# Performance work log

Hardware: AMD Instinct MI355X
Metric: run time of the kernel (lower is better)

## Reference

```python
import jax, jax.numpy as jnp
import numpy as np

DEPTH = 6
HIDDEN = 1152
INTER = 4304
HEADS = 16
HEAD_DIM = HIDDEN // HEADS  # 72
NUM_IMAGES = 4
GH = 32
GW = 32
MERGE = 2
SEQ = NUM_IMAGES * GH * GW  # 4096, cu_seqlens = [0,1024,2048,3072,4096]
OUT_HIDDEN = 2048
NPOS_SIDE = 48
PATCH_DIM = 3 * 2 * 16 * 16  # 1536
DS_IDX = (2, 4)
EPS = 1e-6
SCALE = HEAD_DIM ** -0.5
MERGED = HIDDEN * MERGE * MERGE  # 4608


def _block_order(h, w, m):
    # token order that groups m x m spatial-merge blocks contiguously
    return np.arange(h * w).reshape(h // m, m, w // m, m).transpose(0, 2, 1, 3).reshape(-1)

_ORDER = _block_order(GH, GW, MERGE)


def _rope_cos_sin():
    hpos = _ORDER // GW
    wpos = _ORDER % GW
    half = HEAD_DIM // 2
    inv = 1.0 / (10000.0 ** (np.arange(0, half, 2, dtype=np.float32) / half))
    fr = np.arange(max(GH, GW), dtype=np.float32)[:, None] * inv[None, :]
    r = np.concatenate([fr[hpos], fr[wpos]], axis=-1)  # (GH*GW, head_dim//2)
    emb = np.tile(np.concatenate([r, r], axis=-1), (NUM_IMAGES, 1))  # (SEQ, HEAD_DIM)
    return jnp.asarray(np.cos(emb)), jnp.asarray(np.sin(emb))


def _pos_interp():
    # static bilinear-interp gather indices/weights: 48x48 grid -> (GH,GW), block order
    n = NPOS_SIDE
    hl = np.linspace(0, n - 1, GH); wl = np.linspace(0, n - 1, GW)
    h0 = np.floor(hl).astype(np.int64); h1 = np.minimum(h0 + 1, n - 1); dh = (hl - h0).astype(np.float32)
    w0 = np.floor(wl).astype(np.int64); w1 = np.minimum(w0 + 1, n - 1); dw = (wl - w0).astype(np.float32)
    idx = np.stack([(h0[:, None] * n + w0[None, :]).reshape(-1),
                    (h0[:, None] * n + w1[None, :]).reshape(-1),
                    (h1[:, None] * n + w0[None, :]).reshape(-1),
                    (h1[:, None] * n + w1[None, :]).reshape(-1)], 0)
    wgt = np.stack([((1 - dh)[:, None] * (1 - dw)[None, :]).reshape(-1),
                    ((1 - dh)[:, None] * dw[None, :]).reshape(-1),
                    (dh[:, None] * (1 - dw)[None, :]).reshape(-1),
                    (dh[:, None] * dw[None, :]).reshape(-1)], 0).astype(np.float32)
    return idx[:, _ORDER], wgt[:, _ORDER]

_PIDX, _PWGT = _pos_interp()


def _ln(x, g, b):
    mu = x.mean(-1, keepdims=True)
    var = ((x - mu) ** 2).mean(-1, keepdims=True)
    return (x - mu) * jax.lax.rsqrt(var + EPS) * g + b


def _rot_half(x):
    x1, x2 = jnp.split(x, 2, axis=-1)
    return jnp.concatenate([-x2, x1], axis=-1)


def _attention(x, qkv_w, qkv_b, proj_w, proj_b, cos, sin):
    qkv = (x @ qkv_w.T + qkv_b).reshape(SEQ, 3, HEADS, HEAD_DIM)
    q, k, v = qkv[:, 0], qkv[:, 1], qkv[:, 2]
    c, s = cos[:, None, :], sin[:, None, :]
    q = q * c + _rot_half(q) * s
    k = k * c + _rot_half(k) * s
    # equal-length cu_seqlens chunks -> batched block-diagonal attention
    qb = q.reshape(NUM_IMAGES, -1, HEADS, HEAD_DIM)
    kb = k.reshape(NUM_IMAGES, -1, HEADS, HEAD_DIM)
    vb = v.reshape(NUM_IMAGES, -1, HEADS, HEAD_DIM)
    att = jax.nn.softmax(jnp.einsum('bqhd,bkhd->bhqk', qb, kb) * SCALE, axis=-1)
    o = jnp.einsum('bhqk,bkhd->bqhd', att, vb).reshape(SEQ, HIDDEN)
    return o @ proj_w.T + proj_b


def _merger(x, g, b, f1w, f1b, f2w, f2b, post):
    if post:
        h = _ln(x.reshape(-1, MERGED), g, b)
    else:
        h = _ln(x, g, b).reshape(-1, MERGED)
    h = jax.nn.gelu(h @ f1w.T + f1b, approximate=True)
    return h @ f2w.T + f2b


def setup_inputs():
    key = jax.random.key(0)
    ks = iter(jax.random.split(key, 40))
    def w(shape, scale=0.02):
        return jax.random.normal(next(ks), shape, jnp.float32) * scale
    return {
        'pixel_values': jax.random.normal(next(ks), (SEQ, PATCH_DIM), jnp.float32),
        'patch_w': w((HIDDEN, PATCH_DIM)), 'patch_b': w((HIDDEN,)),
        'pos_embed': w((NPOS_SIDE * NPOS_SIDE, HIDDEN)),
        'qkv_w': w((DEPTH, 3 * HIDDEN, HIDDEN)), 'qkv_b': w((DEPTH, 3 * HIDDEN)),
        'proj_w': w((DEPTH, HIDDEN, HIDDEN)), 'proj_b': w((DEPTH, HIDDEN)),
        'ln1_g': jnp.ones((DEPTH, HIDDEN)), 'ln1_b': jnp.zeros((DEPTH, HIDDEN)),
        'ln2_g': jnp.ones((DEPTH, HIDDEN)), 'ln2_b': jnp.zeros((DEPTH, HIDDEN)),
        'fc1_w': w((DEPTH, INTER, HIDDEN)), 'fc1_b': w((DEPTH, INTER)),
        'fc2_w': w((DEPTH, HIDDEN, INTER)), 'fc2_b': w((DEPTH, HIDDEN)),
        'm_ln_g': jnp.ones((HIDDEN,)), 'm_ln_b': jnp.zeros((HIDDEN,)),
        'm_fc1_w': w((MERGED, MERGED)), 'm_fc1_b': w((MERGED,)),
        'm_fc2_w': w((OUT_HIDDEN, MERGED)), 'm_fc2_b': w((OUT_HIDDEN,)),
        'ds_ln_g': jnp.ones((2, MERGED)), 'ds_ln_b': jnp.zeros((2, MERGED)),
        'ds_fc1_w': w((2, MERGED, MERGED)), 'ds_fc1_b': w((2, MERGED)),
        'ds_fc2_w': w((2, OUT_HIDDEN, MERGED)), 'ds_fc2_b': w((2, OUT_HIDDEN)),
    }


def reference(pixel_values, patch_w, patch_b, pos_embed, qkv_w, qkv_b, proj_w, proj_b,
              ln1_g, ln1_b, ln2_g, ln2_b, fc1_w, fc1_b, fc2_w, fc2_b,
              m_ln_g, m_ln_b, m_fc1_w, m_fc1_b, m_fc2_w, m_fc2_b,
              ds_ln_g, ds_ln_b, ds_fc1_w, ds_fc1_b, ds_fc2_w, ds_fc2_b):
    cos, sin = _rope_cos_sin()
    # patch embed: stride==kernel Conv3d == flat linear on (C*T*P*P)
    x = pixel_values @ patch_w.T + patch_b  # (SEQ, HIDDEN)
    pe = (pos_embed[jnp.asarray(_PIDX)] * jnp.asarray(_PWGT)[..., None]).sum(0)
    x = x + jnp.tile(pe, (NUM_IMAGES, 1))
    ds = []
    for i in range(DEPTH):
        x = x + _attention(_ln(x, ln1_g[i], ln1_b[i]), qkv_w[i], qkv_b[i], proj_w[i], proj_b[i], cos, sin)
        h = _ln(x, ln2_g[i], ln2_b[i])
        x = x + (jax.nn.gelu(h @ fc1_w[i].T + fc1_b[i], approximate=True) @ fc2_w[i].T + fc2_b[i])
        if i in DS_IDX:
            j = DS_IDX.index(i)
            ds.append(_merger(x, ds_ln_g[j], ds_ln_b[j], ds_fc1_w[j], ds_fc1_b[j], ds_fc2_w[j], ds_fc2_b[j], post=True))
    out = _merger(x, m_ln_g, m_ln_b, m_fc1_w, m_fc1_b, m_fc2_w, m_fc2_b, post=False)
    return (out, ds[0], ds[1])
```

## Files before the change

### kernel.cpp

```cpp
#include <hip/hip_runtime.h>
#include <hip/hip_bf16.h>
#include <math.h>

typedef __hip_bfloat16 bf16;
typedef __attribute__((ext_vector_type(8))) __bf16 bfv8;
typedef __attribute__((ext_vector_type(4))) __bf16 bfv4;
typedef __attribute__((ext_vector_type(4))) float float4v;

__device__ inline float bf2f(bf16 v) { return __bfloat162float(v); }
__device__ inline bf16 f2bf(float v) { return __float2bfloat16(v); }

__device__ inline float gelu_f(float v) {
  return 0.5f * v * (1.f + tanhf(0.7978845608028654f * (v + 0.044715f * v * v * v)));
}

__global__ void dtype_probe(const unsigned* __restrict__ g, int* __restrict__ flag) {
  *flag = (*g == 0x3F800000u) ? 1 : 0;
}

__device__ inline float loadf_dyn(const void* p, long i, int isf32) {
  return isf32 ? ((const float*)p)[i] : bf2f(((const bf16*)p)[i]);
}

__global__ __launch_bounds__(256) void cvt_bf16(const void* __restrict__ src,
                                                long off, __bf16* __restrict__ dst,
                                                long n, const int* __restrict__ flagp) {
  const long i = ((long)blockIdx.x * 256 + threadIdx.x) * 8;
  if (i >= n) return;
  if (*flagp) {
    const float* sp = (const float*)src + off + i;
    float4v a = *(const float4v*)sp;
    float4v b = *(const float4v*)(sp + 4);
    bfv8 r;
    r[0] = (__bf16)a[0]; r[1] = (__bf16)a[1];
    r[2] = (__bf16)a[2]; r[3] = (__bf16)a[3];
    r[4] = (__bf16)b[0]; r[5] = (__bf16)b[1];
    r[6] = (__bf16)b[2]; r[7] = (__bf16)b[3];
    *(bfv8*)(dst + i) = r;
  } else {
    *(bfv8*)(dst + i) = *(const bfv8*)((const __bf16*)src + off + i);
  }
}

__device__ inline void cp16(const __bf16* g, __bf16* l) {
  __builtin_amdgcn_global_load_lds(
      (const __attribute__((address_space(1))) void*)g,
      (__attribute__((address_space(3))) void*)l, 16, 0, 0);
}

template <int EPI>
__global__ __launch_bounds__(256) void gemm_bt(
    const void* __restrict__ Av, const void* __restrict__ Wv,
    const void* __restrict__ Bv, void* __restrict__ Cv,
    const int* __restrict__ flagp, int M, int N, int K, int lda, int ldw,
    int ldc, long sA, long sW, long sC, long a0, long w0, long b0, long c0,
    int ksplit, float scale) {
  __shared__ __align__(16) __bf16 As[128 * 32];
  __shared__ __align__(16) __bf16 Ws[128 * 32];
  const int tid = threadIdx.x;
  const int bz = blockIdx.z;

  const int nx = gridDim.x;
  const int nwg = nx * gridDim.y;
  const int orig = blockIdx.y * nx + blockIdx.x;
  const int xcd = orig & 7, lid = orig >> 3, qq = nwg >> 3, rr = nwg & 7;
  const int wg = (xcd < rr ? xcd * (qq + 1) : rr * (qq + 1) + (xcd - rr) * qq) + lid;
  const int bm = (wg / nx) * 128;
  const int bn = (wg % nx) * 128;

  int kof = 0, klen = K;
  if (ksplit > 0) {
    kof = bz * ksplit;
    klen = min(ksplit, K - kof);
  }
  const __bf16* Ap = (const __bf16*)Av + a0 + (size_t)bz * sA + kof;
  const __bf16* Wp = (const __bf16*)Wv + w0 + (size_t)bz * sW + kof;

  const int lane = tid & 63, wid = tid >> 6;
  const int wm = (wid >> 1) * 64, wn = (wid & 1) * 64;
  const int q = lane >> 4, lm = lane & 15;

  const int sr = lane >> 2;
  const int sc = (lane & 3) * 8;
  const int ar = bm + wid * 32 + sr;
  const int wr = bn + wid * 32 + sr;
  const size_t aoff0 = (size_t)(ar < M ? ar : M - 1) * lda + sc;
  const size_t aoff1 = (size_t)(ar + 16 < M ? ar + 16 : M - 1) * lda + sc;
  const size_t woff0 = (size_t)(wr < N ? wr : N - 1) * ldw + sc;
  const size_t woff1 = (size_t)(wr + 16 < N ? wr + 16 : N - 1) * ldw + sc;
  __bf16* lA = &As[wid * 32 * 32];
  __bf16* lW = &Ws[wid * 32 * 32];

  float4v acc[4][4];
#pragma unroll
  for (int i = 0; i < 4; i++)
#pragma unroll
    for (int j = 0; j < 4; j++) acc[i][j] = (float4v)0.f;

  auto compute = [&]() {
    bfv8 af[4], wf[4];
#pragma unroll
    for (int i = 0; i < 4; i++) {
      af[i] = *(const bfv8*)&As[(wm + i * 16 + lm) * 32 + q * 8];
      wf[i] = *(const bfv8*)&Ws[(wn + i * 16 + lm) * 32 + q * 8];
    }
#pragma unroll
    for (int i = 0; i < 4; i++)
#pragma unroll
      for (int j = 0; j < 4; j++)
        acc[i][j] = __builtin_amdgcn_mfma_f32_16x16x32_bf16(af[i], wf[j],
                                                            acc[i][j], 0, 0, 0);
  };

  const int nfull = klen >> 5;
  for (int kt = 0; kt < nfull; ++kt) {
    const int k0 = kt << 5;
    cp16(Ap + aoff0 + k0, lA);
    cp16(Ap + aoff1 + k0, lA + 512);
    cp16(Wp + woff0 + k0, lW);
    cp16(Wp + woff1 + k0, lW + 512);
    __syncthreads();
    compute();
    __syncthreads();
  }

  const int kr = klen & 31;
  if (kr) {
    const int k0 = nfull << 5;
    const int r0 = tid >> 2, ce = (tid & 3) * 8;
#pragma unroll
    for (int it = 0; it < 2; ++it) {
      const int r = r0 + it * 64;
      const int gm = bm + r, gn = bn + r;
      bfv8 av = (bfv8)(__bf16)0.f;
      if (ce < kr && gm < M) av = *(const bfv8*)(Ap + (size_t)gm * lda + k0 + ce);
      *(bfv8*)&As[r * 32 + ce] = av;
      bfv8 wv = (bfv8)(__bf16)0.f;
      if (ce < kr && gn < N) wv = *(const bfv8*)(Wp + (size_t)gn * ldw + k0 + ce);
      *(bfv8*)&Ws[r * 32 + ce] = wv;
    }
    __syncthreads();
    compute();
  }

  const int isf32 = *flagp;
  float* Cf = (float*)Cv;
  bf16* Cb = (bf16*)Cv;
  const size_t cbase = (size_t)c0 + (size_t)bz * sC;
#pragma unroll
  for (int i = 0; i < 4; i++) {
#pragma unroll
    for (int j = 0; j < 4; j++) {
      const int col = bn + wn + j * 16 + lm;
      if (col >= N) continue;
      float bv = 0.f;
      if (EPI != 4 && Bv) bv = loadf_dyn(Bv, b0 + col, isf32);
#pragma unroll
      for (int r = 0; r < 4; r++) {
        const int rowg = bm + wm + i * 16 + q * 4 + r;
        if (rowg >= M) continue;
        float v = acc[i][j][r] + bv;
        const size_t off = cbase + (size_t)rowg * ldc + col;
        if (EPI == 0) {
          Cb[off] = f2bf(v);
        } else if (EPI == 1) {
          Cb[off] = f2bf(gelu_f(v));
        } else if (EPI == 3) {
          Cf[off] = v;
        } else if (EPI == 4) {
          Cf[off] = v * scale;
        }
      }
    }
  }
}

template <int MODE>
__global__ __launch_bounds__(256) void reduce_add(
    const float* __restrict__ part, long slab, int S,
    const void* __restrict__ bias, long b0, void* __restrict__ outv, long c0,
    long n, int N, const int* __restrict__ flagp) {
  const int isf32 = *flagp;
  const long i4 = ((long)blockIdx.x * 256 + threadIdx.x) * 4;
  if (i4 >= n) return;
  float4v s = *(const float4v*)(part + i4);
  for (int t = 1; t < S; ++t) s += *(const float4v*)(part + (size_t)t * slab + i4);
  const int col = (int)(i4 % N);
#pragma unroll
  for (int u = 0; u < 4; ++u) s[u] += loadf_dyn(bias, b0 + col + u, isf32);
  if (MODE == 0) {
    *(float4v*)((float*)outv + i4) = s;
  } else if (MODE == 1) {
    float4v x0 = *(const float4v*)((float*)outv + i4);
    *(float4v*)((float*)outv + i4) = x0 + s;
  } else if (MODE == 2) {
    bfv4 r;
#pragma unroll
    for (int u = 0; u < 4; ++u) r[u] = (__bf16)gelu_f(s[u]);
    *(bfv4*)((bf16*)outv + i4) = r;
  } else {
    if (isf32) {
      *(float4v*)((float*)outv + c0 + i4) = s;
    } else {
      bfv4 r;
#pragma unroll
      for (int u = 0; u < 4; ++u) r[u] = (__bf16)s[u];
      *(bfv4*)((bf16*)outv + c0 + i4) = r;
    }
  }
}

__global__ __launch_bounds__(256) void ln_rows(const float* __restrict__ x,
                                               const void* __restrict__ g,
                                               const void* __restrict__ b,
                                               long gboff, bf16* __restrict__ out,
                                               int C, const int* __restrict__ flagp) {
  const int isf32 = *flagp;
  const int row = blockIdx.x;
  const float* xp = x + (size_t)row * C;
  const int tid = threadIdx.x;
  float s = 0.f, ss = 0.f;
  for (int c = tid; c < C; c += 256) {
    float v = xp[c];
    s += v;
    ss += v * v;
  }
#pragma unroll
  for (int off = 32; off >= 1; off >>= 1) {
    s += __shfl_xor(s, off);
    ss += __shfl_xor(ss, off);
  }
  __shared__ float rs_[4], rss_[4];
  const int wid = tid >> 6;
  if ((tid & 63) == 0) {
    rs_[wid] = s;
    rss_[wid] = ss;
  }
  __syncthreads();
  s = rs_[0] + rs_[1] + rs_[2] + rs_[3];
  ss = rss_[0] + rss_[1] + rss_[2] + rss_[3];
  const float mu = s / C;
  const float var = ss / C - mu * mu;
  const float rstd = rsqrtf(var + 1e-6f);
  bf16* op = out + (size_t)row * C;
  for (int c = tid; c < C; c += 256)
    op[c] = f2bf((xp[c] - mu) * rstd * loadf_dyn(g, gboff + c, isf32) +
                 loadf_dyn(b, gboff + c, isf32));
}

__global__ __launch_bounds__(256) void pe_add(const void* __restrict__ pos,
                                              float* __restrict__ x,
                                              const int* __restrict__ flagp) {
  const int isf32 = *flagp;
  const int idx = blockIdx.x * 256 + threadIdx.x;
  const int h = idx % 1152;
  const int p = idx / 1152;
  const int j = p & 1, i2 = (p >> 1) & 1, bw = (p >> 2) & 15, bh = p >> 6;
  const int hpos = bh * 2 + i2, wpos = bw * 2 + j;
  const double hv = hpos * 47.0 / 31.0, wv = wpos * 47.0 / 31.0;
  const int h0 = (int)hv, w0 = (int)wv;
  const int h1 = min(h0 + 1, 47), w1 = min(w0 + 1, 47);
  const float dh = (float)(hv - h0), dw = (float)(wv - w0);
  const float pe =
      (1.f - dh) * (1.f - dw) * loadf_dyn(pos, (long)(h0 * 48 + w0) * 1152 + h, isf32) +
      (1.f - dh) * dw * loadf_dyn(pos, (long)(h0 * 48 + w1) * 1152 + h, isf32) +
      dh * (1.f - dw) * loadf_dyn(pos, (long)(h1 * 48 + w0) * 1152 + h, isf32) +
      dh * dw * loadf_dyn(pos, (long)(h1 * 48 + w1) * 1152 + h, isf32);
#pragma unroll
  for (int img = 0; img < 4; ++img)
    x[((size_t)(img * 1024 + p)) * 1152 + h] += pe;
}

__global__ __launch_bounds__(256) void rope_split(const bf16* __restrict__ qkv,
                                                  bf16* __restrict__ qb,
                                                  bf16* __restrict__ kb,
                                                  bf16* __restrict__ vt) {
  const int idx = blockIdx.x * 256 + threadIdx.x;
  const int d = idx % 72;
  const int sh = idx / 72;
  const int hh = sh & 15;
  const int s = sh >> 4;
  const int p = s & 1023, img = s >> 10;
  const int jj = p & 1, ii = (p >> 1) & 1, bw = (p >> 2) & 15, bh = p >> 6;
  const int hpos = 2 * bh + ii, wpos = 2 * bw + jj;
  const int dd = (d < 36) ? d : d - 36;
  int t, posv;
  if (dd < 18) { t = dd; posv = hpos; }
  else { t = dd - 18; posv = wpos; }
  const float ang = posv * powf(10000.f, -(2.f * t) / 36.f);
  const float c = cosf(ang), sn = sinf(ang);
  const size_t base = (size_t)s * 3456 + hh * 72;
  const int d2 = (d < 36) ? d + 36 : d - 36;
  const float qv = bf2f(qkv[base + d]);
  const float q2 = bf2f(qkv[base + d2]);
  const float kv = bf2f(qkv[base + 1152 + d]);
  const float k2 = bf2f(qkv[base + 1152 + d2]);
  const float qr = (d < 36) ? qv * c - q2 * sn : qv * c + q2 * sn;
  const float kr = (d < 36) ? kv * c - k2 * sn : kv * c + k2 * sn;
  const size_t ob = (size_t)s * 1152 + hh * 72 + d;
  qb[ob] = f2bf(qr);
  kb[ob] = f2bf(kr);
  vt[(((size_t)(img * 16 + hh)) * 72 + d) * 1024 + p] = qkv[base + 2304 + d];
}

__global__ __launch_bounds__(256) void softmax_rows(const float* __restrict__ S,
                                                    bf16* __restrict__ P) {
  const size_t row = blockIdx.x;
  const float* sp = S + row * 1024;
  const int tid = threadIdx.x;
  float v[4];
  float m = -1e30f;
#pragma unroll
  for (int i = 0; i < 4; i++) {
    v[i] = sp[tid + (i << 8)];
    m = fmaxf(m, v[i]);
  }
#pragma unroll
  for (int off = 32; off >= 1; off >>= 1) m = fmaxf(m, __shfl_xor(m, off));
  __shared__ float red[8];
  const int wid = tid >> 6;
  if ((tid & 63) == 0) red[wid] = m;
  __syncthreads();
  m = fmaxf(fmaxf(red[0], red[1]), fmaxf(red[2], red[3]));
  float s = 0.f;
#pragma unroll
  for (int i = 0; i < 4; i++) {
    v[i] = expf(v[i] - m);
    s += v[i];
  }
#pragma unroll
  for (int off = 32; off >= 1; off >>= 1) s += __shfl_xor(s, off);
  if ((tid & 63) == 0) red[4 + wid] = s;
  __syncthreads();
  s = red[4] + red[5] + red[6] + red[7];
  const float inv = 1.f / s;
  bf16* pp = P + row * 1024;
#pragma unroll
  for (int i = 0; i < 4; i++) pp[tid + (i << 8)] = f2bf(v[i] * inv);
}

extern "C" void kernel_launch(void* const* d_in, const int* in_sizes, int n_in,
                              void* d_out, int out_size, void* d_ws,
                              size_t ws_size, hipStream_t stream) {
  const void* pixel = d_in[0];
  const void* patch_w = d_in[1];
  const void* patch_b = d_in[2];
  const void* pos_emb = d_in[3];
  const void* qkv_w = d_in[4];
  const void* qkv_b = d_in[5];
  const void* proj_w = d_in[6];
  const void* proj_b = d_in[7];
  const void* ln1_g = d_in[8];
  const void* ln1_b = d_in[9];
  const void* ln2_g = d_in[10];
  const void* ln2_b = d_in[11];
  const void* fc1_w = d_in[12];
  const void* fc1_b = d_in[13];
  const void* fc2_w = d_in[14];
  const void* fc2_b = d_in[15];
  const void* m_ln_g = d_in[16];
  const void* m_ln_b = d_in[17];
  const void* m_fc1_w = d_in[18];
  const void* m_fc1_b = d_in[19];
  const void* m_fc2_w = d_in[20];
  const void* m_fc2_b = d_in[21];
  const void* ds_ln_g = d_in[22];
  const void* ds_ln_b = d_in[23];
  const void* ds_fc1_w = d_in[24];
  const void* ds_fc1_b = d_in[25];
  const void* ds_fc2_w = d_in[26];
  const void* ds_fc2_b = d_in[27];

  char* wp = (char*)d_ws;
  auto alloc = [&](size_t bytes) -> char* {
    char* r = wp;
    wp += (bytes + 255) & ~(size_t)255;
    return r;
  };
  int* flag = (int*)alloc(256);
  float* x = (float*)alloc(4718592ull * 4);
  bf16* a_bf = (bf16*)alloc(4718592ull * 2);
  bf16* qkvb = (bf16*)alloc(14155776ull * 2);
  bf16* qb = (bf16*)alloc(4718592ull * 2);
  bf16* kb = (bf16*)alloc(4718592ull * 2);
  bf16* vt = (bf16*)alloc(4718592ull * 2);
  bf16* o_bf = (bf16*)alloc(4718592ull * 2);
  float* sbuf = (float*)alloc(16777216ull * 4);
  bf16* h_bf = (bf16*)alloc(17629184ull * 2);
  bf16* p_bf = h_bf;
  __bf16* wcv = (__bf16*)sbuf;
  __bf16* pix_bf = wcv;
  __bf16* pw_bf = wcv + 8388608;
  float* part = (float*)qkvb;
  const long SLAB = 4718592;

  const dim3 blk(256);
  auto gg = [](int N, int M, int S) {
    return dim3((unsigned)((N + 127) / 128), (unsigned)((M + 127) / 128), (unsigned)S);
  };
  auto cvt = [&](const void* s, long off, __bf16* d, long n) {
    cvt_bf16<<<dim3((unsigned)((n / 8 + 255) / 256)), blk, 0, stream>>>(s, off, d, n, flag);
  };
  auto rgrid = [](long n) { return dim3((unsigned)((n / 4 + 255) / 256)); };
  const float SCALE = 0.11785113019775793f;

  dtype_probe<<<1, 1, 0, stream>>>((const unsigned*)ln1_g, flag);

  cvt(pixel, 0, pix_bf, 6291456);
  cvt(patch_w, 0, pw_bf, 1769472);
  gemm_bt<3><<<gg(1152, 4096, 3), blk, 0, stream>>>(
      pix_bf, pw_bf, nullptr, part, flag, 4096, 1152, 1536, 1536, 1536, 1152,
      0, 0, SLAB, 0, 0, 0, 0, 512, 1.f);
  reduce_add<0><<<rgrid(4718592), blk, 0, stream>>>(
      part, SLAB, 3, patch_b, 0, (void*)x, 0, 4718592, 1152, flag);
  pe_add<<<4608, 256, 0, stream>>>(pos_emb, x, flag);

  for (long L = 0; L < 6; ++L) {
    ln_rows<<<4096, 256, 0, stream>>>(x, ln1_g, ln1_b, L * 1152, a_bf, 1152, flag);
    cvt(qkv_w, L * 3981312L, wcv, 3981312);
    gemm_bt<0><<<gg(3456, 4096, 1), blk, 0, stream>>>(
        a_bf, wcv, qkv_b, qkvb, flag, 4096, 3456, 1152, 1152, 1152, 3456, 0,
        0, 0, 0, 0, L * 3456, 0, 0, 1.f);
    rope_split<<<18432, 256, 0, stream>>>(qkvb, qb, kb, vt);
    for (int img = 0; img < 4; ++img) {
      gemm_bt<4><<<dim3(8, 8, 16), blk, 0, stream>>>(
          qb + (size_t)img * 1179648, kb + (size_t)img * 1179648, nullptr,
          (void*)sbuf, flag, 1024, 1024, 72, 1152, 1152, 1024, 72, 72, 1048576,
          0, 0, 0, 0, 0, SCALE);
      softmax_rows<<<16384, 256, 0, stream>>>(sbuf, p_bf);
      gemm_bt<0><<<dim3(1, 8, 16), blk, 0, stream>>>(
          p_bf, vt + (size_t)img * 1179648, nullptr,
          (void*)(o_bf + (size_t)img * 1179648), flag, 1024, 72, 1024, 1024,
          1024, 1152, 1048576, 73728, 72, 0, 0, 0, 0, 0, 1.f);
    }
    cvt(proj_w, L * 1327104L, wcv, 1327104);
    gemm_bt<3><<<gg(1152, 4096, 3), blk, 0, stream>>>(
        o_bf, wcv, nullptr, part, flag, 4096, 1152, 1152, 1152, 1152, 1152,
        0, 0, SLAB, 0, 0, 0, 0, 384, 1.f);
    reduce_add<1><<<rgrid(4718592), blk, 0, stream>>>(
        part, SLAB, 3, proj_b, L * 1152, (void*)x, 0, 4718592, 1152, flag);

    ln_rows<<<4096, 256, 0, stream>>>(x, ln2_g, ln2_b, L * 1152, a_bf, 1152, flag);
    cvt(fc1_w, L * 4958208L, wcv, 4958208);
    gemm_bt<1><<<gg(4304, 4096, 1), blk, 0, stream>>>(
        a_bf, wcv, fc1_b, h_bf, flag, 4096, 4304, 1152, 1152, 1152, 4304, 0,
        0, 0, 0, 0, L * 4304, 0, 0, 1.f);
    cvt(fc2_w, L * 4958208L, wcv, 4958208);
    gemm_bt<3><<<gg(1152, 4096, 3), blk, 0, stream>>>(
        h_bf, wcv, nullptr, part, flag, 4096, 1152, 4304, 4304, 4304, 1152,
        0, 0, SLAB, 0, 0, 0, 0, 1440, 1.f);
    reduce_add<1><<<rgrid(4718592), blk, 0, stream>>>(
        part, SLAB, 3, fc2_b, L * 1152, (void*)x, 0, 4718592, 1152, flag);

    if (L == 2 || L == 4) {
      const long j = (L == 2) ? 0 : 1;
      ln_rows<<<1024, 256, 0, stream>>>(x, ds_ln_g, ds_ln_b, j * 4608, a_bf, 4608, flag);
      cvt(ds_fc1_w, j * 21233664L, wcv, 21233664);
      gemm_bt<3><<<gg(4608, 1024, 3), blk, 0, stream>>>(
          a_bf, wcv, nullptr, part, flag, 1024, 4608, 4608, 4608, 4608, 4608,
          0, 0, SLAB, 0, 0, 0, 0, 1536, 1.f);
      reduce_add<2><<<rgrid(4718592), blk, 0, stream>>>(
          part, SLAB, 3, ds_fc1_b, j * 4608, h_bf, 0, 4718592, 4608, flag);
      cvt(ds_fc2_w, j * 9437184L, wcv, 9437184);
      gemm_bt<3><<<gg(2048, 1024, 4), blk, 0, stream>>>(
          h_bf, wcv, nullptr, part, flag, 1024, 2048, 4608, 4608, 4608, 2048,
          0, 0, 2097152, 0, 0, 0, 0, 1152, 1.f);
      reduce_add<3><<<rgrid(2097152), blk, 0, stream>>>(
          part, 2097152, 4, ds_fc2_b, j * 2048, d_out, (1 + j) * 2097152L,
          2097152, 2048, flag);
    }
  }
  ln_rows<<<4096, 256, 0, stream>>>(x, m_ln_g, m_ln_b, 0, a_bf, 1152, flag);
  cvt(m_fc1_w, 0, wcv, 21233664);
  gemm_bt<3><<<gg(4608, 1024, 3), blk, 0, stream>>>(
      a_bf, wcv, nullptr, part, flag, 1024, 4608, 4608, 4608, 4608, 4608,
      0, 0, SLAB, 0, 0, 0, 0, 1536, 1.f);
  reduce_add<2><<<rgrid(4718592), blk, 0, stream>>>(
      part, SLAB, 3, m_fc1_b, 0, h_bf, 0, 4718592, 4608, flag);
  cvt(m_fc2_w, 0, wcv, 9437184);
  gemm_bt<3><<<gg(2048, 1024, 4), blk, 0, stream>>>(
      h_bf, wcv, nullptr, part, flag, 1024, 2048, 4608, 4608, 4608, 2048,
      0, 0, 2097152, 0, 0, 0, 0, 1152, 1.f);
  reduce_add<3><<<rgrid(2097152), blk, 0, stream>>>(
      part, 2097152, 4, m_fc2_b, 0, d_out, 0, 2097152, 2048, flag);
}
```

Baseline: 5.544 ms.

## Double-buffer GEMM LDS tiles and split-K the attention PV GEMM

Result: faster. 5.063 ms (-8.7%).

```diff
diff --git a/kernel.cpp b/kernel.cpp
--- a/kernel.cpp
+++ b/kernel.cpp
@@ -54,9 +54,9 @@
     const void* __restrict__ Bv, void* __restrict__ Cv,
     const int* __restrict__ flagp, int M, int N, int K, int lda, int ldw,
     int ldc, long sA, long sW, long sC, long a0, long w0, long b0, long c0,
-    int ksplit, float scale) {
-  __shared__ __align__(16) __bf16 As[128 * 32];
-  __shared__ __align__(16) __bf16 Ws[128 * 32];
+    int ksplit, int zheads, long slabC, float scale) {
+  __shared__ __align__(16) __bf16 As[2][128 * 32];
+  __shared__ __align__(16) __bf16 Ws[2][128 * 32];
   const int tid = threadIdx.x;
   const int bz = blockIdx.z;
 
@@ -68,13 +68,15 @@
   const int bm = (wg / nx) * 128;
   const int bn = (wg % nx) * 128;
 
-  int kof = 0, klen = K;
+  int head = bz, ks = 0, kof = 0, klen = K;
   if (ksplit > 0) {
-    kof = bz * ksplit;
+    head = bz % zheads;
+    ks = bz / zheads;
+    kof = ks * ksplit;
     klen = min(ksplit, K - kof);
   }
-  const __bf16* Ap = (const __bf16*)Av + a0 + (size_t)bz * sA + kof;
-  const __bf16* Wp = (const __bf16*)Wv + w0 + (size_t)bz * sW + kof;
+  const __bf16* Ap = (const __bf16*)Av + a0 + (size_t)head * sA + kof;
+  const __bf16* Wp = (const __bf16*)Wv + w0 + (size_t)head * sW + kof;
 
   const int lane = tid & 63, wid = tid >> 6;
   const int wm = (wid >> 1) * 64, wn = (wid & 1) * 64;
@@ -88,8 +90,6 @@
   const size_t aoff1 = (size_t)(ar + 16 < M ? ar + 16 : M - 1) * lda + sc;
   const size_t woff0 = (size_t)(wr < N ? wr : N - 1) * ldw + sc;
   const size_t woff1 = (size_t)(wr + 16 < N ? wr + 16 : N - 1) * ldw + sc;
-  __bf16* lA = &As[wid * 32 * 32];
-  __bf16* lW = &Ws[wid * 32 * 32];
 
   float4v acc[4][4];
 #pragma unroll
@@ -97,35 +97,19 @@
 #pragma unroll
     for (int j = 0; j < 4; j++) acc[i][j] = (float4v)0.f;
 
-  auto compute = [&]() {
-    bfv8 af[4], wf[4];
-#pragma unroll
-    for (int i = 0; i < 4; i++) {
-      af[i] = *(const bfv8*)&As[(wm + i * 16 + lm) * 32 + q * 8];
-      wf[i] = *(const bfv8*)&Ws[(wn + i * 16 + lm) * 32 + q * 8];
-    }
-#pragma unroll
-    for (int i = 0; i < 4; i++)
-#pragma unroll
-      for (int j = 0; j < 4; j++)
-        acc[i][j] = __builtin_amdgcn_mfma_f32_16x16x32_bf16(af[i], wf[j],
-                                                            acc[i][j], 0, 0, 0);
-  };
-
   const int nfull = klen >> 5;
-  for (int kt = 0; kt < nfull; ++kt) {
+  const int kr = klen & 31;
+
+  auto stage = [&](int buf, int kt) {
     const int k0 = kt << 5;
+    __bf16* lA = &As[buf][wid * 1024];
+    __bf16* lW = &Ws[buf][wid * 1024];
     cp16(Ap + aoff0 + k0, lA);
     cp16(Ap + aoff1 + k0, lA + 512);
     cp16(Wp + woff0 + k0, lW);
     cp16(Wp + woff1 + k0, lW + 512);
-    __syncthreads();
-    compute();
-    __syncthreads();
-  }
-
-  const int kr = klen & 31;
-  if (kr) {
+  };
+  auto stage_tail = [&](int buf) {
     const int k0 = nfull << 5;
     const int r0 = tid >> 2, ce = (tid & 3) * 8;
 #pragma unroll
@@ -134,19 +118,46 @@
       const int gm = bm + r, gn = bn + r;
       bfv8 av = (bfv8)(__bf16)0.f;
       if (ce < kr && gm < M) av = *(const bfv8*)(Ap + (size_t)gm * lda + k0 + ce);
-      *(bfv8*)&As[r * 32 + ce] = av;
+      *(bfv8*)&As[buf][r * 32 + ce] = av;
       bfv8 wv = (bfv8)(__bf16)0.f;
       if (ce < kr && gn < N) wv = *(const bfv8*)(Wp + (size_t)gn * ldw + k0 + ce);
-      *(bfv8*)&Ws[r * 32 + ce] = wv;
+      *(bfv8*)&Ws[buf][r * 32 + ce] = wv;
     }
+  };
+  auto compute = [&](int buf) {
+    bfv8 af[4], wf[4];
+#pragma unroll
+    for (int i = 0; i < 4; i++) {
+      af[i] = *(const bfv8*)&As[buf][(wm + i * 16 + lm) * 32 + q * 8];
+      wf[i] = *(const bfv8*)&Ws[buf][(wn + i * 16 + lm) * 32 + q * 8];
+    }
+    __builtin_amdgcn_s_setprio(1);
+#pragma unroll
+    for (int i = 0; i < 4; i++)
+#pragma unroll
+      for (int j = 0; j < 4; j++)
+        acc[i][j] = __builtin_amdgcn_mfma_f32_16x16x32_bf16(af[i], wf[j],
+                                                            acc[i][j], 0, 0, 0);
+    __builtin_amdgcn_s_setprio(0);
+  };
+
+  int cur = 0;
+  if (nfull > 0) stage(0, 0);
+  else if (kr) stage_tail(0);
+  __syncthreads();
+  for (int kt = 0; kt < nfull; ++kt) {
+    if (kt + 1 < nfull) stage(cur ^ 1, kt + 1);
+    else if (kr) stage_tail(cur ^ 1);
+    compute(cur);
     __syncthreads();
-    compute();
-  }
+    cur ^= 1;
+  }
+  if (kr) compute(cur);
 
   const int isf32 = *flagp;
   float* Cf = (float*)Cv;
   bf16* Cb = (bf16*)Cv;
-  const size_t cbase = (size_t)c0 + (size_t)bz * sC;
+  const size_t cbase = (size_t)c0 + (size_t)head * sC + (size_t)ks * slabC;
 #pragma unroll
   for (int i = 0; i < 4; i++) {
 #pragma unroll
@@ -185,6 +196,17 @@
   if (i4 >= n) return;
   float4v s = *(const float4v*)(part + i4);
   for (int t = 1; t < S; ++t) s += *(const float4v*)(part + (size_t)t * slab + i4);
+  if (MODE == 4) {
+    const long z = i4 / 73728;
+    const long rem = i4 % 73728;
+    const long row = rem / 72;
+    const long col = rem % 72;
+    bfv4 r;
+#pragma unroll
+    for (int u = 0; u < 4; ++u) r[u] = (__bf16)s[u];
+    *(bfv4*)((bf16*)outv + row * 1152 + z * 72 + col) = r;
+    return;
+  }
   const int col = (int)(i4 % N);
 #pragma unroll
   for (int u = 0; u < 4; ++u) s[u] += loadf_dyn(bias, b0 + col + u, isf32);
@@ -410,7 +432,7 @@
   cvt(patch_w, 0, pw_bf, 1769472);
   gemm_bt<3><<<gg(1152, 4096, 3), blk, 0, stream>>>(
       pix_bf, pw_bf, nullptr, part, flag, 4096, 1152, 1536, 1536, 1536, 1152,
-      0, 0, SLAB, 0, 0, 0, 0, 512, 1.f);
+      0, 0, 0, 0, 0, 0, 0, 512, 1, SLAB, 1.f);
   reduce_add<0><<<rgrid(4718592), blk, 0, stream>>>(
       part, SLAB, 3, patch_b, 0, (void*)x, 0, 4718592, 1152, flag);
   pe_add<<<4608, 256, 0, stream>>>(pos_emb, x, flag);
@@ -420,23 +442,26 @@
     cvt(qkv_w, L * 3981312L, wcv, 3981312);
     gemm_bt<0><<<gg(3456, 4096, 1), blk, 0, stream>>>(
         a_bf, wcv, qkv_b, qkvb, flag, 4096, 3456, 1152, 1152, 1152, 3456, 0,
-        0, 0, 0, 0, L * 3456, 0, 0, 1.f);
+        0, 0, 0, 0, L * 3456, 0, 0, 1, 0, 1.f);
     rope_split<<<18432, 256, 0, stream>>>(qkvb, qb, kb, vt);
     for (int img = 0; img < 4; ++img) {
       gemm_bt<4><<<dim3(8, 8, 16), blk, 0, stream>>>(
           qb + (size_t)img * 1179648, kb + (size_t)img * 1179648, nullptr,
           (void*)sbuf, flag, 1024, 1024, 72, 1152, 1152, 1024, 72, 72, 1048576,
-          0, 0, 0, 0, 0, SCALE);
+          0, 0, 0, 0, 0, 1, 0, SCALE);
       softmax_rows<<<16384, 256, 0, stream>>>(sbuf, p_bf);
-      gemm_bt<0><<<dim3(1, 8, 16), blk, 0, stream>>>(
-          p_bf, vt + (size_t)img * 1179648, nullptr,
-          (void*)(o_bf + (size_t)img * 1179648), flag, 1024, 72, 1024, 1024,
-          1024, 1152, 1048576, 73728, 72, 0, 0, 0, 0, 0, 1.f);
+      gemm_bt<3><<<dim3(1, 8, 64), blk, 0, stream>>>(
+          p_bf, vt + (size_t)img * 1179648, nullptr, part, flag, 1024, 72,
+          1024, 1024, 1024, 72, 1048576, 73728, 73728, 0, 0, 0, 0, 256, 16,
+          1179648, 1.f);
+      reduce_add<4><<<rgrid(1179648), blk, 0, stream>>>(
+          part, 1179648, 4, nullptr, 0, (void*)(o_bf + (size_t)img * 1179648),
+          0, 1179648, 72, flag);
     }
     cvt(proj_w, L * 1327104L, wcv, 1327104);
     gemm_bt<3><<<gg(1152, 4096, 3), blk, 0, stream>>>(
         o_bf, wcv, nullptr, part, flag, 4096, 1152, 1152, 1152, 1152, 1152,
-        0, 0, SLAB, 0, 0, 0, 0, 384, 1.f);
+        0, 0, 0, 0, 0, 0, 0, 384, 1, SLAB, 1.f);
     reduce_add<1><<<rgrid(4718592), blk, 0, stream>>>(
         part, SLAB, 3, proj_b, L * 1152, (void*)x, 0, 4718592, 1152, flag);
 
@@ -444,11 +469,11 @@
     cvt(fc1_w, L * 4958208L, wcv, 4958208);
     gemm_bt<1><<<gg(4304, 4096, 1), blk, 0, stream>>>(
         a_bf, wcv, fc1_b, h_bf, flag, 4096, 4304, 1152, 1152, 1152, 4304, 0,
-        0, 0, 0, 0, L * 4304, 0, 0, 1.f);
+        0, 0, 0, 0, L * 4304, 0, 0, 1, 0, 1.f);
     cvt(fc2_w, L * 4958208L, wcv, 4958208);
     gemm_bt<3><<<gg(1152, 4096, 3), blk, 0, stream>>>(
         h_bf, wcv, nullptr, part, flag, 4096, 1152, 4304, 4304, 4304, 1152,
-        0, 0, SLAB, 0, 0, 0, 0, 1440, 1.f);
+        0, 0, 0, 0, 0, 0, 0, 1440, 1, SLAB, 1.f);
     reduce_add<1><<<rgrid(4718592), blk, 0, stream>>>(
         part, SLAB, 3, fc2_b, L * 1152, (void*)x, 0, 4718592, 1152, flag);
 
@@ -458,13 +483,13 @@
       cvt(ds_fc1_w, j * 21233664L, wcv, 21233664);
       gemm_bt<3><<<gg(4608, 1024, 3), blk, 0, stream>>>(
           a_bf, wcv, nullptr, part, flag, 1024, 4608, 4608, 4608, 4608, 4608,
-          0, 0, SLAB, 0, 0, 0, 0, 1536, 1.f);
+          0, 0, 0, 0, 0, 0, 0, 1536, 1, SLAB, 1.f);
       reduce_add<2><<<rgrid(4718592), blk, 0, stream>>>(
           part, SLAB, 3, ds_fc1_b, j * 4608, h_bf, 0, 4718592, 4608, flag);
       cvt(ds_fc2_w, j * 9437184L, wcv, 9437184);
       gemm_bt<3><<<gg(2048, 1024, 4), blk, 0, stream>>>(
           h_bf, wcv, nullptr, part, flag, 1024, 2048, 4608, 4608, 4608, 2048,
-          0, 0, 2097152, 0, 0, 0, 0, 1152, 1.f);
+          0, 0, 0, 0, 0, 0, 0, 1152, 1, 2097152, 1.f);
       reduce_add<3><<<rgrid(2097152), blk, 0, stream>>>(
           part, 2097152, 4, ds_fc2_b, j * 2048, d_out, (1 + j) * 2097152L,
           2097152, 2048, flag);
@@ -474,13 +499,13 @@
   cvt(m_fc1_w, 0, wcv, 21233664);
   gemm_bt<3><<<gg(4608, 1024, 3), blk, 0, stream>>>(
       a_bf, wcv, nullptr, part, flag, 1024, 4608, 4608, 4608, 4608, 4608,
-      0, 0, SLAB, 0, 0, 0, 0, 1536, 1.f);
+      0, 0, 0, 0, 0, 0, 0, 1536, 1, SLAB, 1.f);
   reduce_add<2><<<rgrid(4718592), blk, 0, stream>>>(
       part, SLAB, 3, m_fc1_b, 0, h_bf, 0, 4718592, 4608, flag);
   cvt(m_fc2_w, 0, wcv, 9437184);
   gemm_bt<3><<<gg(2048, 1024, 4), blk, 0, stream>>>(
       h_bf, wcv, nullptr, part, flag, 1024, 2048, 4608, 4608, 4608, 2048,
-      0, 0, 2097152, 0, 0, 0, 0, 1152, 1.f);
+      0, 0, 0, 0, 0, 0, 0, 1152, 1, 2097152, 1.f);
   reduce_add<3><<<rgrid(2097152), blk, 0, stream>>>(
       part, 2097152, 4, m_fc2_b, 0, d_out, 0, 2097152, 2048, flag);
 }
```
